# Kernel optimization log

Hardware: AMD Instinct MI355X
Metric: run time of the kernel (lower is better)

Reference implementation:

```python
import jax, jax.numpy as jnp
import numpy as np

N_PARTIAL = 1024  # matches init_kwargs


def setup_inputs() -> dict:
    key = jax.random.key(0)
    k1, k2 = jax.random.split(key)
    B, H, L = 8, 768, 4096
    x = jax.random.normal(k1, (B, H, L), dtype=jnp.float32)
    k = jax.random.normal(k2, (H, L), dtype=jnp.float32)
    return {"x": x, "k": k}


def reference(x, k):
    # FFT-based causal long convolution with low-pass frequency truncation.
    L = x.shape[-1]
    N = 2 * L  # zero-pad to 2L for linear (non-circular) convolution
    x_dtype = x.dtype
    x_f = jnp.fft.rfft(x.astype(jnp.float32), n=N)          # [B, H, N//2+1] complex64
    k_f = jnp.fft.rfft(k.astype(jnp.float32), n=N)          # [H, N//2+1]   complex64
    # zero out all frequency bins >= N_partial // 2 (low-pass truncation of the kernel)
    freqs = jnp.arange(N // 2 + 1)
    k_f = jnp.where(freqs < N_PARTIAL // 2, k_f, jnp.zeros((), dtype=k_f.dtype))
    y_f = x_f * k_f                                          # broadcast over batch
    y = jnp.fft.irfft(y_f, n=N)[..., :L].astype(x_dtype)     # [B, H, L]
    return y
```

## Files before the change

kernel.cpp:

```cpp
#include <hip/hip_runtime.h>
#include <math.h>

#define LSEQ 4096
#define NFFT 8192
#define NF   512
#define NF2  1024
#define NH   768
#define NBH  6144
#define MROWS 6912
#define SPLIT_ROW 3584

typedef __attribute__((ext_vector_type(8))) short short8;
typedef __attribute__((ext_vector_type(4))) float floatx4;

__device__ __forceinline__ unsigned short f2bf(float f) {
    unsigned int u = __float_as_uint(f);
    u += 0x7fff + ((u >> 16) & 1);
    return (unsigned short)(u >> 16);
}

__device__ __forceinline__ void gld16(const unsigned short* g, const unsigned short* l) {
    __builtin_amdgcn_global_load_lds(
        (const __attribute__((address_space(1))) void*)g,
        (__attribute__((address_space(3))) void*)l, 16, 0, 0);
}

__global__ void build_tables(unsigned short* __restrict__ T1,
                             unsigned short* __restrict__ T2) {
    __shared__ unsigned short tile[64][66];
    const int t = threadIdx.x;
    const int F0 = blockIdx.x * 64;
    const int N0 = blockIdx.y * 64;
#pragma unroll
    for (int i = 0; i < 16; ++i) {
        int r = (t >> 6) + i * 4;
        int c = t & 63;
        int f2 = F0 + r, n = N0 + c;
        int f = f2 >> 1;
        int p = (f * n) & (NFFT - 1);
        float th = (float)p * (float)(2.0 * M_PI / (double)NFFT);
        float s, cc;
        sincosf(th, &s, &cc);
        unsigned short v = f2bf((f2 & 1) ? s : cc);
        T1[(size_t)f2 * LSEQ + n] = v;
        tile[r][c] = v;
    }
    __syncthreads();
#pragma unroll
    for (int i = 0; i < 16; ++i) {
        int r = (t >> 6) + i * 4;
        int c = t & 63;
        T2[(size_t)(N0 + r) * NF2 + F0 + c] = tile[c][r];
    }
}

__global__ void tobf16(const float* __restrict__ x, const float* __restrict__ kk,
                       unsigned short* __restrict__ o) {
    size_t e = ((size_t)blockIdx.x * 256 + threadIdx.x) * 4;
    const size_t XN = (size_t)NBH * LSEQ;
    const float* s = (e < XN) ? (x + e) : (kk + (e - XN));
    float4 v = *(const float4*)s;
    unsigned int lo = (unsigned int)f2bf(v.x) | ((unsigned int)f2bf(v.y) << 16);
    unsigned int hi = (unsigned int)f2bf(v.z) | ((unsigned int)f2bf(v.w) << 16);
    *(uint2*)(o + e) = make_uint2(lo, hi);
}

__global__ __launch_bounds__(512) void gemm8(
    const unsigned short* __restrict__ A,
    const unsigned short* __restrict__ B,
    float* __restrict__ C,
    float* __restrict__ P1a,
    float* __restrict__ P1b,
    int gx, int gy, int N, int ldk, int Ksub)
{
    __shared__ __align__(16) unsigned short S[2 * 32768];
    const int t = threadIdx.x;
    const int wid = t >> 6, l = t & 63;

    const int nwg = gridDim.x, bid = blockIdx.x;
    const int swz = (bid & 7) * (nwg >> 3) + (bid >> 3);
    const int bx = swz % gx;
    const int rem = swz / gx;
    const int by = rem % gy;
    const int bz = rem / gy;

    const int m0 = by * 256, n0 = bx * 256;
    const int wr = wid >> 2, wc = wid & 3;
    const int lq = l >> 4, lr = l & 15;
    const int kbase = bz * Ksub;
    const int NT = Ksub >> 6;

    const int s0 = lq ^ (lr & 7);
    const int aoff = (wr * 128 + lr) * 64 + s0 * 8;
    const int boff = 16384 + (wc * 64 + lr) * 64 + s0 * 8;

    const int gsl = (l & 7) ^ ((l >> 3) & 7);
    const unsigned short* pAs = A + (size_t)(m0 + wid * 8 + (l >> 3)) * ldk + kbase + gsl * 8;
    const unsigned short* pBs = B + (size_t)(n0 + wid * 8 + (l >> 3)) * ldk + kbase + gsl * 8;

    floatx4 acc[8][4];
#pragma unroll
    for (int i = 0; i < 8; ++i)
#pragma unroll
        for (int j = 0; j < 4; ++j)
            acc[i][j] = (floatx4){0.f, 0.f, 0.f, 0.f};

#define STG_TILE(b, kt_)                                                                   \
    gld16(pAs + (size_t)  0 * ldk + (kt_) * 64, S + (b)*32768 +         (  0 + wid*8) * 64); \
    gld16(pAs + (size_t) 64 * ldk + (kt_) * 64, S + (b)*32768 +         ( 64 + wid*8) * 64); \
    gld16(pAs + (size_t)128 * ldk + (kt_) * 64, S + (b)*32768 +         (128 + wid*8) * 64); \
    gld16(pAs + (size_t)192 * ldk + (kt_) * 64, S + (b)*32768 +         (192 + wid*8) * 64); \
    gld16(pBs + (size_t)  0 * ldk + (kt_) * 64, S + (b)*32768 + 16384 + (  0 + wid*8) * 64); \
    gld16(pBs + (size_t) 64 * ldk + (kt_) * 64, S + (b)*32768 + 16384 + ( 64 + wid*8) * 64); \
    gld16(pBs + (size_t)128 * ldk + (kt_) * 64, S + (b)*32768 + 16384 + (128 + wid*8) * 64); \
    gld16(pBs + (size_t)192 * ldk + (kt_) * 64, S + (b)*32768 + 16384 + (192 + wid*8) * 64);

#define RD_A(Sc, ip)                                                           \
    _Pragma("unroll") for (int ii = 0; ii < 2; ++ii)                           \
    _Pragma("unroll") for (int ks = 0; ks < 2; ++ks)                           \
        aq[ii][ks] = *(const short8*)((Sc) + ((aoff ^ (ks * 32)) + 1024 * ((ip) + ii)));
#define RD_B(Sc)                                                               \
    _Pragma("unroll") for (int j = 0; j < 4; ++j)                              \
    _Pragma("unroll") for (int ks = 0; ks < 2; ++ks)                           \
        bq[j][ks] = *(const short8*)((Sc) + ((boff ^ (ks * 32)) + 1024 * j));
#define MM(ip)                                                                 \
    __builtin_amdgcn_s_setprio(1);                                             \
    _Pragma("unroll") for (int ii = 0; ii < 2; ++ii)                           \
    _Pragma("unroll") for (int j = 0; j < 4; ++j)                              \
    _Pragma("unroll") for (int ks = 0; ks < 2; ++ks)                           \
        acc[(ip) + ii][j] = __builtin_amdgcn_mfma_f32_16x16x32_bf16(           \
            aq[ii][ks], bq[j][ks], acc[(ip) + ii][j], 0, 0, 0);                \
    __builtin_amdgcn_s_setprio(0);

    STG_TILE(0, 0)
    asm volatile("s_waitcnt vmcnt(0)" ::: "memory");
    __builtin_amdgcn_s_barrier();
    __builtin_amdgcn_sched_barrier(0);

    short8 aq[2][2], bq[4][2];

    for (int kt = 0; kt < NT; ++kt) {
        const unsigned short* Sc = S + (size_t)(kt & 1) * 32768;
        const int bs = (kt & 1) ^ 1;
        const bool pf = (kt + 1 < NT);
        if (pf) { STG_TILE(bs, kt + 1) }
        RD_B(Sc)
        RD_A(Sc, 0) MM(0)
        RD_A(Sc, 2) MM(2)
        RD_A(Sc, 4) MM(4)
        RD_A(Sc, 6) MM(6)
        if (pf) {
            asm volatile("s_waitcnt vmcnt(0)" ::: "memory");
            __builtin_amdgcn_s_barrier();
            __builtin_amdgcn_sched_barrier(0);
        }
    }

    float* Cb;
    if (bz == 0) Cb = C;
    else Cb = (m0 < SPLIT_ROW) ? P1a : (P1b - (size_t)SPLIT_ROW * N);
#pragma unroll
    for (int i = 0; i < 8; ++i)
#pragma unroll
        for (int j = 0; j < 4; ++j)
#pragma unroll
            for (int r = 0; r < 4; ++r) {
                int row = m0 + wr * 128 + 16 * i + lq * 4 + r;
                int col = n0 + wc * 64 + 16 * j + lr;
                Cb[(size_t)row * N + col] = acc[i][j][r];
            }
}

__global__ void combine(const float* __restrict__ C1,
                        const float* __restrict__ P1a,
                        const float* __restrict__ P1b,
                        unsigned short* __restrict__ AB) {
    int idx = blockIdx.x * blockDim.x + threadIdx.x;
    int bh = idx >> 9;
    int f = idx & (NF - 1);
    int h = bh % NH;
    const float* xc = C1 + (size_t)bh * NF2 + 2 * f;
    const float* xp = (bh < SPLIT_ROW)
        ? (P1a + (size_t)bh * NF2 + 2 * f)
        : (P1b + (size_t)(bh - SPLIT_ROW) * NF2 + 2 * f);
    const int kr = NBH + h;
    const float* kc = C1 + (size_t)kr * NF2 + 2 * f;
    const float* kp = P1b + (size_t)(kr - SPLIT_ROW) * NF2 + 2 * f;
    float Xre = xc[0] + xp[0], Xim = -(xc[1] + xp[1]);
    float Kre = kc[0] + kp[0], Kim = -(kc[1] + kp[1]);
    float s = (f == 0 ? 1.0f : 2.0f) * (1.0f / (float)NFFT);
    float Av = s * (Xre * Kre - Xim * Kim);
    float Bv = -(s * (Xre * Kim + Xim * Kre));
    unsigned int packed = (unsigned int)f2bf(Av) | ((unsigned int)f2bf(Bv) << 16);
    *(unsigned int*)(AB + (size_t)bh * NF2 + 2 * f) = packed;
}

extern "C" void kernel_launch(void* const* d_in, const int* in_sizes, int n_in,
                              void* d_out, int out_size, void* d_ws, size_t ws_size,
                              hipStream_t stream) {
    const float* x = (const float*)d_in[0];
    const float* k = (const float*)d_in[1];
    float* y = (float*)d_out;

    unsigned short* T1 = (unsigned short*)d_ws;
    unsigned short* T2 = T1 + (size_t)NF2 * LSEQ;
    unsigned short* AB = T2 + (size_t)LSEQ * NF2;
    float* P1a = (float*)(AB + (size_t)NBH * NF2);

    unsigned short* Abm = (unsigned short*)d_out;
    float* C1 = (float*)((char*)d_out + (size_t)MROWS * LSEQ * 2);
    float* P1b = C1 + (size_t)MROWS * NF2;

    const int blk = 256;
    hipLaunchKernelGGL(build_tables, dim3(NF2 / 64, LSEQ / 64), dim3(blk), 0, stream, T1, T2);
    hipLaunchKernelGGL(tobf16, dim3((MROWS * LSEQ / 4) / blk), dim3(blk), 0, stream, x, k, Abm);
    hipLaunchKernelGGL(gemm8, dim3(4 * 27 * 2), dim3(512), 0, stream,
                       Abm, T1, C1, P1a, P1b, 4, 27, NF2, LSEQ, LSEQ / 2);
    hipLaunchKernelGGL(combine, dim3((NBH * NF) / blk), dim3(blk), 0, stream, C1, P1a, P1b, AB);
    hipLaunchKernelGGL(gemm8, dim3(16 * 24), dim3(512), 0, stream,
                       AB, T2, y, (float*)nullptr, (float*)nullptr, 16, 24, LSEQ, NF2, NF2);
}
```

Baseline: 309.7 us.

## Shrink GEMM tile to 128x256 single-buffered LDS for higher occupancy

The GEMM kernel's M tile shrinks from 256 to 128 rows, accumulators halve, and the LDS double buffer becomes a single buffer. Launch bounds now request 4 blocks per CU. The grids double so more workgroups cover the MI355X CUs, and lower register and LDS use allows more waves per CU. In exchange the explicit prefetch overlap is lost: each k-step waits on its loads before computing, and B-tile reuse per load is lower.

```diff
diff --git a/kernel.cpp b/kernel.cpp
--- a/kernel.cpp
+++ b/kernel.cpp
@@ -65,7 +65,7 @@
     *(uint2*)(o + e) = make_uint2(lo, hi);
 }
 
-__global__ __launch_bounds__(512) void gemm8(
+__global__ __launch_bounds__(512, 4) void gemm1b(
     const unsigned short* __restrict__ A,
     const unsigned short* __restrict__ B,
     float* __restrict__ C,
@@ -73,7 +73,9 @@
     float* __restrict__ P1b,
     int gx, int gy, int N, int ldk, int Ksub)
 {
-    __shared__ __align__(16) unsigned short S[2 * 32768];
+    constexpr int ASZ = 128 * 64;
+    constexpr int BSZ = 256 * 64;
+    __shared__ __align__(16) unsigned short S[ASZ + BSZ];
     const int t = threadIdx.x;
     const int wid = t >> 6, l = t & 63;
 
@@ -84,88 +86,72 @@
     const int by = rem % gy;
     const int bz = rem / gy;
 
-    const int m0 = by * 256, n0 = bx * 256;
+    const int m0 = by * 128, n0 = bx * 256;
     const int wr = wid >> 2, wc = wid & 3;
     const int lq = l >> 4, lr = l & 15;
     const int kbase = bz * Ksub;
     const int NT = Ksub >> 6;
 
     const int s0 = lq ^ (lr & 7);
-    const int aoff = (wr * 128 + lr) * 64 + s0 * 8;
-    const int boff = 16384 + (wc * 64 + lr) * 64 + s0 * 8;
+    const int aoff = (wr * 64 + lr) * 64 + s0 * 8;
+    const int boff = ASZ + (wc * 64 + lr) * 64 + s0 * 8;
 
     const int gsl = (l & 7) ^ ((l >> 3) & 7);
     const unsigned short* pAs = A + (size_t)(m0 + wid * 8 + (l >> 3)) * ldk + kbase + gsl * 8;
     const unsigned short* pBs = B + (size_t)(n0 + wid * 8 + (l >> 3)) * ldk + kbase + gsl * 8;
 
-    floatx4 acc[8][4];
-#pragma unroll
-    for (int i = 0; i < 8; ++i)
+    floatx4 acc[4][4];
+#pragma unroll
+    for (int i = 0; i < 4; ++i)
 #pragma unroll
         for (int j = 0; j < 4; ++j)
             acc[i][j] = (floatx4){0.f, 0.f, 0.f, 0.f};
 
-#define STG_TILE(b, kt_)                                                                   \
-    gld16(pAs + (size_t)  0 * ldk + (kt_) * 64, S + (b)*32768 +         (  0 + wid*8) * 64); \
-    gld16(pAs + (size_t) 64 * ldk + (kt_) * 64, S + (b)*32768 +         ( 64 + wid*8) * 64); \
-    gld16(pAs + (size_t)128 * ldk + (kt_) * 64, S + (b)*32768 +         (128 + wid*8) * 64); \
-    gld16(pAs + (size_t)192 * ldk + (kt_) * 64, S + (b)*32768 +         (192 + wid*8) * 64); \
-    gld16(pBs + (size_t)  0 * ldk + (kt_) * 64, S + (b)*32768 + 16384 + (  0 + wid*8) * 64); \
-    gld16(pBs + (size_t) 64 * ldk + (kt_) * 64, S + (b)*32768 + 16384 + ( 64 + wid*8) * 64); \
-    gld16(pBs + (size_t)128 * ldk + (kt_) * 64, S + (b)*32768 + 16384 + (128 + wid*8) * 64); \
-    gld16(pBs + (size_t)192 * ldk + (kt_) * 64, S + (b)*32768 + 16384 + (192 + wid*8) * 64);
-
-#define RD_A(Sc, ip)                                                           \
-    _Pragma("unroll") for (int ii = 0; ii < 2; ++ii)                           \
-    _Pragma("unroll") for (int ks = 0; ks < 2; ++ks)                           \
-        aq[ii][ks] = *(const short8*)((Sc) + ((aoff ^ (ks * 32)) + 1024 * ((ip) + ii)));
-#define RD_B(Sc)                                                               \
-    _Pragma("unroll") for (int j = 0; j < 4; ++j)                              \
-    _Pragma("unroll") for (int ks = 0; ks < 2; ++ks)                           \
-        bq[j][ks] = *(const short8*)((Sc) + ((boff ^ (ks * 32)) + 1024 * j));
-#define MM(ip)                                                                 \
-    __builtin_amdgcn_s_setprio(1);                                             \
-    _Pragma("unroll") for (int ii = 0; ii < 2; ++ii)                           \
-    _Pragma("unroll") for (int j = 0; j < 4; ++j)                              \
-    _Pragma("unroll") for (int ks = 0; ks < 2; ++ks)                           \
-        acc[(ip) + ii][j] = __builtin_amdgcn_mfma_f32_16x16x32_bf16(           \
-            aq[ii][ks], bq[j][ks], acc[(ip) + ii][j], 0, 0, 0);                \
-    __builtin_amdgcn_s_setprio(0);
-
-    STG_TILE(0, 0)
-    asm volatile("s_waitcnt vmcnt(0)" ::: "memory");
-    __builtin_amdgcn_s_barrier();
-    __builtin_amdgcn_sched_barrier(0);
-
-    short8 aq[2][2], bq[4][2];
-
     for (int kt = 0; kt < NT; ++kt) {
-        const unsigned short* Sc = S + (size_t)(kt & 1) * 32768;
-        const int bs = (kt & 1) ^ 1;
-        const bool pf = (kt + 1 < NT);
-        if (pf) { STG_TILE(bs, kt + 1) }
-        RD_B(Sc)
-        RD_A(Sc, 0) MM(0)
-        RD_A(Sc, 2) MM(2)
-        RD_A(Sc, 4) MM(4)
-        RD_A(Sc, 6) MM(6)
-        if (pf) {
-            asm volatile("s_waitcnt vmcnt(0)" ::: "memory");
-            __builtin_amdgcn_s_barrier();
-            __builtin_amdgcn_sched_barrier(0);
+#pragma unroll
+        for (int h = 0; h < 2; ++h)
+            gld16(pAs + (size_t)(64 * h) * ldk + kt * 64, S + (64 * h + wid * 8) * 64);
+#pragma unroll
+        for (int h = 0; h < 4; ++h)
+            gld16(pBs + (size_t)(64 * h) * ldk + kt * 64, S + ASZ + (64 * h + wid * 8) * 64);
+        asm volatile("s_waitcnt vmcnt(0)" ::: "memory");
+        __builtin_amdgcn_s_barrier();
+        __builtin_amdgcn_sched_barrier(0);
+
+        short8 bq[4][2];
+#pragma unroll
+        for (int j = 0; j < 4; ++j)
+#pragma unroll
+            for (int ks = 0; ks < 2; ++ks)
+                bq[j][ks] = *(const short8*)(S + ((boff ^ (ks * 32)) + 1024 * j));
+#pragma unroll
+        for (int i = 0; i < 4; ++i) {
+            short8 aq[2];
+#pragma unroll
+            for (int ks = 0; ks < 2; ++ks)
+                aq[ks] = *(const short8*)(S + ((aoff ^ (ks * 32)) + 1024 * i));
+            __builtin_amdgcn_s_setprio(1);
+#pragma unroll
+            for (int j = 0; j < 4; ++j)
+#pragma unroll
+                for (int ks = 0; ks < 2; ++ks)
+                    acc[i][j] = __builtin_amdgcn_mfma_f32_16x16x32_bf16(
+                        aq[ks], bq[j][ks], acc[i][j], 0, 0, 0);
+            __builtin_amdgcn_s_setprio(0);
         }
+        __builtin_amdgcn_s_barrier();
     }
 
     float* Cb;
     if (bz == 0) Cb = C;
     else Cb = (m0 < SPLIT_ROW) ? P1a : (P1b - (size_t)SPLIT_ROW * N);
 #pragma unroll
-    for (int i = 0; i < 8; ++i)
+    for (int i = 0; i < 4; ++i)
 #pragma unroll
         for (int j = 0; j < 4; ++j)
 #pragma unroll
             for (int r = 0; r < 4; ++r) {
-                int row = m0 + wr * 128 + 16 * i + lq * 4 + r;
+                int row = m0 + wr * 64 + 16 * i + lq * 4 + r;
                 int col = n0 + wc * 64 + 16 * j + lr;
                 Cb[(size_t)row * N + col] = acc[i][j][r];
             }
@@ -214,9 +200,9 @@
     const int blk = 256;
     hipLaunchKernelGGL(build_tables, dim3(NF2 / 64, LSEQ / 64), dim3(blk), 0, stream, T1, T2);
     hipLaunchKernelGGL(tobf16, dim3((MROWS * LSEQ / 4) / blk), dim3(blk), 0, stream, x, k, Abm);
-    hipLaunchKernelGGL(gemm8, dim3(4 * 27 * 2), dim3(512), 0, stream,
-                       Abm, T1, C1, P1a, P1b, 4, 27, NF2, LSEQ, LSEQ / 2);
+    hipLaunchKernelGGL(gemm1b, dim3(4 * 54 * 2), dim3(512), 0, stream,
+                       Abm, T1, C1, P1a, P1b, 4, 54, NF2, LSEQ, LSEQ / 2);
     hipLaunchKernelGGL(combine, dim3((NBH * NF) / blk), dim3(blk), 0, stream, C1, P1a, P1b, AB);
-    hipLaunchKernelGGL(gemm8, dim3(16 * 24), dim3(512), 0, stream,
-                       AB, T2, y, (float*)nullptr, (float*)nullptr, 16, 24, LSEQ, NF2, NF2);
-}
+    hipLaunchKernelGGL(gemm1b, dim3(16 * 48), dim3(512), 0, stream,
+                       AB, T2, y, (float*)nullptr, (float*)nullptr, 16, 48, LSEQ, NF2, NF2);
+}
```

New measurement: 312.3 us. About the same (+0.8%).
